# Performance work log

Measured on AMD Instinct MI355X. Metric: run time of the kernel, lower is better.

The kernel has to match this reference:

```python
import jax, jax.numpy as jnp
import numpy as np

B, T, H = 65536, 24, 64  # batch, input_window_size, num_neurons
SLOPE = 25.0             # snntorch fast_sigmoid default slope

@jax.custom_vjp
def spike(x):
    # heaviside forward, fast-sigmoid surrogate backward
    return (x > 0).astype(x.dtype)

def _spike_fwd(x):
    return (x > 0).astype(x.dtype), x

def _spike_bwd(x, g):
    return (g / (SLOPE * jnp.abs(x) + 1.0) ** 2,)

spike.defvjp(_spike_fwd, _spike_bwd)

def slstm_cell(x, syn, mem, Wih, Whh, bih, bhh, thr):
    # snntorch SLSTM: LSTMCell with h=mem, c=syn; reset_mechanism='subtract'
    reset = jax.lax.stop_gradient((mem - thr > 0).astype(x.dtype))
    gates = x @ Wih.T + bih + mem @ Whh.T + bhh  # (B, 4H)
    i, f, g, o = jnp.split(gates, 4, axis=-1)
    syn_new = jax.nn.sigmoid(f) * syn + jax.nn.sigmoid(i) * jnp.tanh(g)
    mem_new = jax.nn.sigmoid(o) * jnp.tanh(syn_new) - reset * thr
    spk = spike(mem_new - thr)
    return spk, syn_new, mem_new

def setup_inputs() -> dict:
    key = jax.random.key(0)
    ks = jax.random.split(key, 11)
    s = float(1.0 / np.sqrt(H))  # LSTMCell uniform init bound
    so = float(1.0 / np.sqrt((T + 2) * H))
    u = lambda k, shape: jax.random.uniform(k, shape, jnp.float32, -s, s)
    return {
        "x": jax.random.normal(ks[0], (B, T, 1), jnp.float32),
        "Wih1": u(ks[1], (4 * H, 1)),
        "Whh1": u(ks[2], (4 * H, H)),
        "bih1": u(ks[3], (4 * H,)),
        "bhh1": u(ks[4], (4 * H,)),
        "thr1": jnp.float32(0.5),
        "Wih2": u(ks[5], (4 * H, H)),
        "Whh2": u(ks[6], (4 * H, H)),
        "bih2": u(ks[7], (4 * H,)),
        "bhh2": u(ks[8], (4 * H,)),
        "thr2": jnp.float32(0.5),
        "Wout": jax.random.uniform(ks[9], (2, (T + 2) * H), jnp.float32, -so, so),
        "bout": jnp.array([0.2, -0.2], jnp.float32),
    }

def reference(x, Wih1, Whh1, bih1, bhh1, thr1,
              Wih2, Whh2, bih2, bhh2, thr2, Wout, bout):
    Bn = x.shape[0]
    Hn = Whh1.shape[1]
    z = jnp.zeros((Bn, Hn), x.dtype)
    carry0 = (z, z, z, z)  # syn1, mem1, syn2, mem2

    def step(carry, xt):
        syn1, mem1, syn2, mem2 = carry
        spk1, syn1, mem1 = slstm_cell(xt, syn1, mem1, Wih1, Whh1, bih1, bhh1, thr1)
        spk2, syn2, mem2 = slstm_cell(spk1, syn2, mem2, Wih2, Whh2, bih2, bhh2, thr2)
        return (syn1, mem1, syn2, mem2), spk2

    (syn1, mem1, syn2, mem2), spk2_seq = jax.lax.scan(
        step, carry0, jnp.swapaxes(x, 0, 1))  # spk2_seq: (T, B, H)
    # extra step: feed mem1 into slstm2
    spk2_last, syn2, mem2 = slstm_cell(mem1, syn2, mem2, Wih2, Whh2, bih2, bhh2, thr2)
    lst = jnp.concatenate(
        [jnp.swapaxes(spk2_seq, 0, 1).reshape(Bn, -1), spk2_last, mem2], axis=1)
    return lst @ Wout.T + bout  # (B, 2)
```

## Files before the change

### kernel.cpp

```cpp
#include <hip/hip_runtime.h>
#include <cstdint>
#include <cstddef>


#define BB 65536
#define TT 24
#define NB 8

typedef float pf2 __attribute__((ext_vector_type(2)));

__device__ __forceinline__ void pk_fma_wlo(pf2& acc, pf2 s, pf2 w) {
  asm("v_pk_fma_f32 %0, %1, %2, %0 op_sel:[0,0,0] op_sel_hi:[1,0,1]"
      : "+v"(acc) : "v"(s), "v"(w));
}
__device__ __forceinline__ void pk_fma_whi(pf2& acc, pf2 s, pf2 w) {
  asm("v_pk_fma_f32 %0, %1, %2, %0 op_sel:[0,1,0] op_sel_hi:[1,1,1]"
      : "+v"(acc) : "v"(s), "v"(w));
}

__device__ __forceinline__ float bcastf(float v, int l) {
  return __int_as_float(__builtin_amdgcn_readlane(__float_as_int(v), l));
}
__device__ __forceinline__ float sigm(float v) {
  return __fdividef(1.0f, 1.0f + __expf(-v));
}
__device__ __forceinline__ float tanh_fast(float v) {
  return fmaf(-2.0f, __fdividef(1.0f, __expf(2.0f * v) + 1.0f), 1.0f);
}
__device__ __forceinline__ float wsum(float v) {
#pragma unroll
  for (int o = 32; o > 0; o >>= 1) v += __shfl_xor(v, o);
  return v;
}

__global__ __attribute__((amdgpu_waves_per_eu(4, 4))) __launch_bounds__(512)
void snn_pass1(
    const float* __restrict__ x, const float* __restrict__ Wih1,
    const float* __restrict__ Whh1, const float* __restrict__ bih1,
    const float* __restrict__ bhh1, const float* __restrict__ thr1p,
    unsigned long long* __restrict__ spk_out, float* __restrict__ mem1_out) {
  __shared__ float4 P1[64][64];
  __shared__ float stM[8][64][NB];
  int tid = threadIdx.x;
  for (int idx = tid; idx < 16384; idx += 512) {
    int k = idx >> 6, m = idx & 63;
    ((float*)&P1[m][k & 63])[k >> 6] = Whh1[idx];
  }
  __syncthreads();
  int lane = tid & 63, wave = tid >> 6;
  int wb = (blockIdx.x * 8 + wave) * NB;
  float thr1 = thr1p[0];
  float b1q[4], wq[4];
#pragma unroll
  for (int q = 0; q < 4; q++) {
    b1q[q] = bih1[q * 64 + lane] + bhh1[q * 64 + lane];
    wq[q] = Wih1[q * 64 + lane];
  }
  float syn[NB], mem[NB];
#pragma unroll
  for (int b = 0; b < NB; b++) { syn[b] = 0.0f; mem[b] = 0.0f; }

  for (int t = 0; t < TT; t++) {
#pragma unroll
    for (int b = 0; b < NB; b++) stM[wave][lane][b] = mem[b];
    unsigned long long myspk = 0;
#pragma unroll
    for (int h = 0; h < 2; h++) {
      const int B0 = h * 4;
      pf2 a2[4][2];
#pragma unroll
      for (int p = 0; p < 2; p++) {
        float x0 = x[(wb + B0 + 2 * p) * TT + t];
        float x1 = x[(wb + B0 + 2 * p + 1) * TT + t];
#pragma unroll
        for (int q = 0; q < 4; q++)
          a2[q][p] = (pf2){fmaf(x0, wq[q], b1q[q]), fmaf(x1, wq[q], b1q[q])};
      }
#pragma unroll 8
      for (int m = 0; m < 64; m++) {
        float4 w = P1[m][lane];
        float4 sa = *(const float4*)&stM[wave][m][B0];
        pf2 s01 = {sa.x, sa.y}, s23 = {sa.z, sa.w};
        pf2 wxy = {w.x, w.y}, wzw = {w.z, w.w};
        pk_fma_wlo(a2[0][0], s01, wxy);
        pk_fma_whi(a2[1][0], s01, wxy);
        pk_fma_wlo(a2[2][0], s01, wzw);
        pk_fma_whi(a2[3][0], s01, wzw);
        pk_fma_wlo(a2[0][1], s23, wxy);
        pk_fma_whi(a2[1][1], s23, wxy);
        pk_fma_wlo(a2[2][1], s23, wzw);
        pk_fma_whi(a2[3][1], s23, wzw);
      }
#pragma unroll
      for (int j = 0; j < 4; j++) {
        int b = B0 + j, p = j >> 1;
        float aq0 = (j & 1) ? a2[0][p].y : a2[0][p].x;
        float aq1 = (j & 1) ? a2[1][p].y : a2[1][p].x;
        float aq2 = (j & 1) ? a2[2][p].y : a2[2][p].x;
        float aq3 = (j & 1) ? a2[3][p].y : a2[3][p].x;
        float ig = sigm(aq0), fg = sigm(aq1);
        float gg = tanh_fast(aq2), og = sigm(aq3);
        float sn = fmaf(fg, syn[b], ig * gg);
        float rst = (mem[b] > thr1) ? thr1 : 0.0f;
        float mn = fmaf(og, tanh_fast(sn), -rst);
        syn[b] = sn;
        mem[b] = mn;
        unsigned long long msk = __ballot(mn > thr1);
        if (lane == b) myspk = msk;
      }
      __builtin_amdgcn_sched_barrier(0);
    }
    if (lane < NB)
      spk_out[(size_t)t * BB + wb + lane] = myspk;
  }
#pragma unroll
  for (int b = 0; b < NB; b++)
    mem1_out[(size_t)(wb + b) * 64 + lane] = mem[b];
}

__global__ __attribute__((amdgpu_waves_per_eu(4, 4))) __launch_bounds__(1024)
void snn_pass2(
    const float* __restrict__ Wih2, const float* __restrict__ Whh2,
    const float* __restrict__ bih2, const float* __restrict__ bhh2,
    const float* __restrict__ thr2p, const float* __restrict__ Wout,
    const float* __restrict__ bout,
    const unsigned long long* __restrict__ spk_in,
    const float* __restrict__ mem1_in, float* __restrict__ out) {
  __shared__ float4 Pih[64][64];
  __shared__ float4 Phh[64][64];
  __shared__ float stM[16][64][NB];
  int tid = threadIdx.x;
  for (int idx = tid; idx < 16384; idx += 1024) {
    int k = idx >> 6, m = idx & 63;
    ((float*)&Pih[m][k & 63])[k >> 6] = Wih2[idx];
    ((float*)&Phh[m][k & 63])[k >> 6] = Whh2[idx];
  }
  __syncthreads();
  int lane = tid & 63, wave = tid >> 6;
  int wb = (blockIdx.x * 16 + wave) * NB;
  float thr2 = thr2p[0];
  float b2q[4];
#pragma unroll
  for (int q = 0; q < 4; q++) b2q[q] = bih2[q * 64 + lane] + bhh2[q * 64 + lane];
  float syn[NB], mem[NB];
  unsigned sb8[NB];
#pragma unroll
  for (int b = 0; b < NB; b++) { syn[b] = 0.0f; mem[b] = 0.0f; sb8[b] = 0u; }

  for (int t = 0; t < TT; t++) {
    unsigned long long mk[NB];
#pragma unroll
    for (int b = 0; b < NB; b++) {
      unsigned long long v = spk_in[(size_t)t * BB + wb + b];
      unsigned lo = __builtin_amdgcn_readfirstlane((unsigned)v);
      unsigned hi = __builtin_amdgcn_readfirstlane((unsigned)(v >> 32));
      mk[b] = ((unsigned long long)hi << 32) | (unsigned long long)lo;
    }
#pragma unroll
    for (int b = 0; b < NB; b++) stM[wave][lane][b] = mem[b];
#pragma unroll
    for (int h = 0; h < 2; h++) {
      const int B0 = h * 4;
      pf2 a2[4][2];
#pragma unroll
      for (int q = 0; q < 4; q++) {
#pragma unroll
        for (int p = 0; p < 2; p++) a2[q][p] = (pf2){b2q[q], b2q[q]};
      }
#pragma unroll 8
      for (int m = 0; m < 64; m++) {
        float4 wh = Phh[m][lane];
        float4 sa = *(const float4*)&stM[wave][m][B0];
        pf2 s01 = {sa.x, sa.y}, s23 = {sa.z, sa.w};
        pf2 wxy = {wh.x, wh.y}, wzw = {wh.z, wh.w};
        pk_fma_wlo(a2[0][0], s01, wxy);
        pk_fma_whi(a2[1][0], s01, wxy);
        pk_fma_wlo(a2[2][0], s01, wzw);
        pk_fma_whi(a2[3][0], s01, wzw);
        pk_fma_wlo(a2[0][1], s23, wxy);
        pk_fma_whi(a2[1][1], s23, wxy);
        pk_fma_wlo(a2[2][1], s23, wzw);
        pk_fma_whi(a2[3][1], s23, wzw);
      }
#pragma unroll
      for (int j = 0; j < 4; j++) {
        int b = B0 + j, p = j >> 1;
        unsigned long long k = mk[b];
        while (__builtin_popcountll(k) >= 4) {
          int m0 = __builtin_ctzll(k); k &= k - 1;
          int m1 = __builtin_ctzll(k); k &= k - 1;
          int m2 = __builtin_ctzll(k); k &= k - 1;
          int m3 = __builtin_ctzll(k); k &= k - 1;
          float4 r0 = Pih[m0][lane];
          float4 r1 = Pih[m1][lane];
          float4 r2 = Pih[m2][lane];
          float4 r3 = Pih[m3][lane];
          if ((j & 1) == 0) {
            a2[0][p].x += r0.x; a2[1][p].x += r0.y; a2[2][p].x += r0.z; a2[3][p].x += r0.w;
            a2[0][p].x += r1.x; a2[1][p].x += r1.y; a2[2][p].x += r1.z; a2[3][p].x += r1.w;
            a2[0][p].x += r2.x; a2[1][p].x += r2.y; a2[2][p].x += r2.z; a2[3][p].x += r2.w;
            a2[0][p].x += r3.x; a2[1][p].x += r3.y; a2[2][p].x += r3.z; a2[3][p].x += r3.w;
          } else {
            a2[0][p].y += r0.x; a2[1][p].y += r0.y; a2[2][p].y += r0.z; a2[3][p].y += r0.w;
            a2[0][p].y += r1.x; a2[1][p].y += r1.y; a2[2][p].y += r1.z; a2[3][p].y += r1.w;
            a2[0][p].y += r2.x; a2[1][p].y += r2.y; a2[2][p].y += r2.z; a2[3][p].y += r2.w;
            a2[0][p].y += r3.x; a2[1][p].y += r3.y; a2[2][p].y += r3.z; a2[3][p].y += r3.w;
          }
        }
        while (k) {
          int m0 = __builtin_ctzll(k); k &= k - 1;
          float4 r0 = Pih[m0][lane];
          if ((j & 1) == 0) {
            a2[0][p].x += r0.x; a2[1][p].x += r0.y; a2[2][p].x += r0.z; a2[3][p].x += r0.w;
          } else {
            a2[0][p].y += r0.x; a2[1][p].y += r0.y; a2[2][p].y += r0.z; a2[3][p].y += r0.w;
          }
        }
        float aq0 = (j & 1) ? a2[0][p].y : a2[0][p].x;
        float aq1 = (j & 1) ? a2[1][p].y : a2[1][p].x;
        float aq2 = (j & 1) ? a2[2][p].y : a2[2][p].x;
        float aq3 = (j & 1) ? a2[3][p].y : a2[3][p].x;
        float ig = sigm(aq0), fg = sigm(aq1);
        float gg = tanh_fast(aq2), og = sigm(aq3);
        float sn = fmaf(fg, syn[b], ig * gg);
        float rst = (mem[b] > thr2) ? thr2 : 0.0f;
        float mn = fmaf(og, tanh_fast(sn), -rst);
        syn[b] = sn;
        mem[b] = mn;
        sb8[b] |= (mn > thr2) ? (1u << t) : 0u;
      }
      __builtin_amdgcn_sched_barrier(0);
    }
  }

  float m1[NB];
#pragma unroll
  for (int b = 0; b < NB; b++) m1[b] = mem1_in[(size_t)(wb + b) * 64 + lane];
  float acc[NB][4];
#pragma unroll
  for (int b = 0; b < NB; b++) {
#pragma unroll
    for (int q = 0; q < 4; q++) acc[b][q] = b2q[q];
  }
#pragma unroll 4
  for (int m = 0; m < 64; m++) {
    float4 wi = Pih[m][lane];
    float4 wh = Phh[m][lane];
#pragma unroll
    for (int b = 0; b < NB; b++) {
      float s1 = bcastf(m1[b], m);
      float s2 = bcastf(mem[b], m);
      acc[b][0] = fmaf(s1, wi.x, fmaf(s2, wh.x, acc[b][0]));
      acc[b][1] = fmaf(s1, wi.y, fmaf(s2, wh.y, acc[b][1]));
      acc[b][2] = fmaf(s1, wi.z, fmaf(s2, wh.z, acc[b][2]));
      acc[b][3] = fmaf(s1, wi.w, fmaf(s2, wh.w, acc[b][3]));
    }
  }
  float p0[NB], p1[NB];
#pragma unroll
  for (int b = 0; b < NB; b++) { p0[b] = 0.0f; p1[b] = 0.0f; }
#pragma unroll 4
  for (int t = 0; t < TT; t++) {
    float w0 = Wout[t * 64 + lane];
    float w1 = Wout[1664 + t * 64 + lane];
#pragma unroll
    for (int b = 0; b < NB; b++) {
      float sf = ((sb8[b] >> t) & 1u) ? 1.0f : 0.0f;
      p0[b] = fmaf(sf, w0, p0[b]);
      p1[b] = fmaf(sf, w1, p1[b]);
    }
  }
  float wA0 = Wout[1536 + lane], wA1 = Wout[1664 + 1536 + lane];
  float wB0 = Wout[1600 + lane], wB1 = Wout[1664 + 1600 + lane];
  float bo0 = bout[0], bo1 = bout[1];
#pragma unroll
  for (int b = 0; b < NB; b++) {
    float ig = sigm(acc[b][0]), fg = sigm(acc[b][1]);
    float gg = tanh_fast(acc[b][2]), og = sigm(acc[b][3]);
    float sn = fmaf(fg, syn[b], ig * gg);
    float rst = (mem[b] > thr2) ? thr2 : 0.0f;
    float mn = fmaf(og, tanh_fast(sn), -rst);
    float sf = (mn > thr2) ? 1.0f : 0.0f;
    p0[b] = fmaf(sf, wA0, p0[b]);
    p1[b] = fmaf(sf, wA1, p1[b]);
    p0[b] = fmaf(mn, wB0, p0[b]);
    p1[b] = fmaf(mn, wB1, p1[b]);
  }
  float vout = 0.0f;
#pragma unroll
  for (int b = 0; b < NB; b++) {
    float r0 = wsum(p0[b]);
    float r1 = wsum(p1[b]);
    if (lane == 2 * b) vout = r0;
    if (lane == 2 * b + 1) vout = r1;
  }
  if (lane < 2 * NB)
    out[(size_t)wb * 2 + lane] = vout + ((lane & 1) ? bo1 : bo0);
}

extern "C" void kernel_launch(void* const* d_in, const int* in_sizes, int n_in,
                              void* d_out, int out_size, void* d_ws, size_t ws_size,
                              hipStream_t stream) {
  const float* x = (const float*)d_in[0];
  const float* Wih1 = (const float*)d_in[1];
  const float* Whh1 = (const float*)d_in[2];
  const float* bih1 = (const float*)d_in[3];
  const float* bhh1 = (const float*)d_in[4];
  const float* thr1 = (const float*)d_in[5];
  const float* Wih2 = (const float*)d_in[6];
  const float* Whh2 = (const float*)d_in[7];
  const float* bih2 = (const float*)d_in[8];
  const float* bhh2 = (const float*)d_in[9];
  const float* thr2 = (const float*)d_in[10];
  const float* Wout = (const float*)d_in[11];
  const float* bout = (const float*)d_in[12];

  unsigned long long* spk = (unsigned long long*)d_ws;
  float* mem1 = (float*)((char*)d_ws + (size_t)TT * BB * 8);

  snn_pass1<<<BB / (8 * NB), 512, 0, stream>>>(x, Wih1, Whh1, bih1, bhh1, thr1,
                                               spk, mem1);
  snn_pass2<<<BB / (16 * NB), 1024, 0, stream>>>(Wih2, Whh2, bih2, bhh2, thr2,
                                                 Wout, bout, spk, mem1,
                                                 (float*)d_out);
}
```

Baseline: 1.776 ms.

## Move half of Whh1 and all of Wih2 weight tables from LDS to global memory

Adds a setup kernel that pre-packs Whh1 and Wih2 into float4-interleaved global buffers. Pass1 now keeps only half of the Whh1 table in LDS and streams the other half from global or cache. Pass2 drops its Pih LDS table and reads Wih2 rows straight from global memory. The goal is to free LDS so more blocks or waves fit per CU, at the cost of global and L1/L2 latency on the inner loops. It also removes the occupancy attribute from pass1 and adds one extra kernel launch.

```diff
diff --git a/kernel.cpp b/kernel.cpp
--- a/kernel.cpp
+++ b/kernel.cpp
@@ -33,18 +33,30 @@
   return v;
 }
 
-__global__ __attribute__((amdgpu_waves_per_eu(4, 4))) __launch_bounds__(512)
-void snn_pass1(
+__global__ void snn_setup(const float* __restrict__ Whh1,
+                          const float* __restrict__ Wih2,
+                          float* __restrict__ P1G, float* __restrict__ PihG) {
+  int idx = blockIdx.x * blockDim.x + threadIdx.x;
+  if (idx < 16384) {
+    int k = idx >> 6, m = idx & 63;
+    int q = k >> 6, j = k & 63;
+    P1G[(m * 64 + j) * 4 + q] = Whh1[idx];
+    PihG[(m * 64 + j) * 4 + q] = Wih2[idx];
+  }
+}
+
+__global__ __launch_bounds__(512) void snn_pass1(
     const float* __restrict__ x, const float* __restrict__ Wih1,
     const float* __restrict__ Whh1, const float* __restrict__ bih1,
     const float* __restrict__ bhh1, const float* __restrict__ thr1p,
+    const float4* __restrict__ P1G,
     unsigned long long* __restrict__ spk_out, float* __restrict__ mem1_out) {
-  __shared__ float4 P1[64][64];
+  __shared__ float4 P1[32][64];
   __shared__ float stM[8][64][NB];
   int tid = threadIdx.x;
   for (int idx = tid; idx < 16384; idx += 512) {
     int k = idx >> 6, m = idx & 63;
-    ((float*)&P1[m][k & 63])[k >> 6] = Whh1[idx];
+    if (m < 32) ((float*)&P1[m][k & 63])[k >> 6] = Whh1[idx];
   }
   __syncthreads();
   int lane = tid & 63, wave = tid >> 6;
@@ -77,8 +89,23 @@
           a2[q][p] = (pf2){fmaf(x0, wq[q], b1q[q]), fmaf(x1, wq[q], b1q[q])};
       }
 #pragma unroll 8
-      for (int m = 0; m < 64; m++) {
+      for (int m = 0; m < 32; m++) {
         float4 w = P1[m][lane];
+        float4 sa = *(const float4*)&stM[wave][m][B0];
+        pf2 s01 = {sa.x, sa.y}, s23 = {sa.z, sa.w};
+        pf2 wxy = {w.x, w.y}, wzw = {w.z, w.w};
+        pk_fma_wlo(a2[0][0], s01, wxy);
+        pk_fma_whi(a2[1][0], s01, wxy);
+        pk_fma_wlo(a2[2][0], s01, wzw);
+        pk_fma_whi(a2[3][0], s01, wzw);
+        pk_fma_wlo(a2[0][1], s23, wxy);
+        pk_fma_whi(a2[1][1], s23, wxy);
+        pk_fma_wlo(a2[2][1], s23, wzw);
+        pk_fma_whi(a2[3][1], s23, wzw);
+      }
+#pragma unroll 8
+      for (int m = 32; m < 64; m++) {
+        float4 w = P1G[m * 64 + lane];
         float4 sa = *(const float4*)&stM[wave][m][B0];
         pf2 s01 = {sa.x, sa.y}, s23 = {sa.z, sa.w};
         pf2 wxy = {w.x, w.y}, wzw = {w.z, w.w};
@@ -123,16 +150,14 @@
     const float* __restrict__ Wih2, const float* __restrict__ Whh2,
     const float* __restrict__ bih2, const float* __restrict__ bhh2,
     const float* __restrict__ thr2p, const float* __restrict__ Wout,
-    const float* __restrict__ bout,
+    const float* __restrict__ bout, const float4* __restrict__ PihG,
     const unsigned long long* __restrict__ spk_in,
     const float* __restrict__ mem1_in, float* __restrict__ out) {
-  __shared__ float4 Pih[64][64];
   __shared__ float4 Phh[64][64];
   __shared__ float stM[16][64][NB];
   int tid = threadIdx.x;
   for (int idx = tid; idx < 16384; idx += 1024) {
     int k = idx >> 6, m = idx & 63;
-    ((float*)&Pih[m][k & 63])[k >> 6] = Wih2[idx];
     ((float*)&Phh[m][k & 63])[k >> 6] = Whh2[idx];
   }
   __syncthreads();
@@ -191,10 +216,10 @@
           int m1 = __builtin_ctzll(k); k &= k - 1;
           int m2 = __builtin_ctzll(k); k &= k - 1;
           int m3 = __builtin_ctzll(k); k &= k - 1;
-          float4 r0 = Pih[m0][lane];
-          float4 r1 = Pih[m1][lane];
-          float4 r2 = Pih[m2][lane];
-          float4 r3 = Pih[m3][lane];
+          float4 r0 = PihG[m0 * 64 + lane];
+          float4 r1 = PihG[m1 * 64 + lane];
+          float4 r2 = PihG[m2 * 64 + lane];
+          float4 r3 = PihG[m3 * 64 + lane];
           if ((j & 1) == 0) {
             a2[0][p].x += r0.x; a2[1][p].x += r0.y; a2[2][p].x += r0.z; a2[3][p].x += r0.w;
             a2[0][p].x += r1.x; a2[1][p].x += r1.y; a2[2][p].x += r1.z; a2[3][p].x += r1.w;
@@ -209,7 +234,7 @@
         }
         while (k) {
           int m0 = __builtin_ctzll(k); k &= k - 1;
-          float4 r0 = Pih[m0][lane];
+          float4 r0 = PihG[m0 * 64 + lane];
           if ((j & 1) == 0) {
             a2[0][p].x += r0.x; a2[1][p].x += r0.y; a2[2][p].x += r0.z; a2[3][p].x += r0.w;
           } else {
@@ -244,7 +269,7 @@
   }
 #pragma unroll 4
   for (int m = 0; m < 64; m++) {
-    float4 wi = Pih[m][lane];
+    float4 wi = PihG[m * 64 + lane];
     float4 wh = Phh[m][lane];
 #pragma unroll
     for (int b = 0; b < NB; b++) {
@@ -317,10 +342,13 @@
 
   unsigned long long* spk = (unsigned long long*)d_ws;
   float* mem1 = (float*)((char*)d_ws + (size_t)TT * BB * 8);
-
+  float* P1G = (float*)((char*)d_ws + (size_t)TT * BB * 8 + (size_t)BB * 64 * 4);
+  float* PihG = P1G + 16384;
+
+  snn_setup<<<32, 512, 0, stream>>>(Whh1, Wih2, P1G, PihG);
   snn_pass1<<<BB / (8 * NB), 512, 0, stream>>>(x, Wih1, Whh1, bih1, bhh1, thr1,
-                                               spk, mem1);
+                                               (const float4*)P1G, spk, mem1);
   snn_pass2<<<BB / (16 * NB), 1024, 0, stream>>>(Wih2, Whh2, bih2, bhh2, thr2,
-                                                 Wout, bout, spk, mem1,
-                                                 (float*)d_out);
-}
+                                                 Wout, bout, (const float4*)PihG,
+                                                 spk, mem1, (float*)d_out);
+}
```

After: 1.871 ms. +5.3%, slower.

## Fuse both SLSTM layers into one kernel and read Wih2 from global memory

Applied to the files above, without the earlier changes.

The two passes are merged into a single kernel. Each wave now computes layer-1 and layer-2 per timestep with all state held in registers, so the spike masks and mem1 no longer round-trip through global memory. A small setup kernel writes Wih2 into a gate-interleaved global layout, and the spike-driven row gathers read from there instead of LDS. This keeps LDS at two weight tables (Whh1, Whh2) plus the state buffer at 1024 threads per block. The cost is that the sparse Wih2 lookups now go through the cache hierarchy rather than LDS, and each thread carries more live registers.

```diff
diff --git a/kernel.cpp b/kernel.cpp
--- a/kernel.cpp
+++ b/kernel.cpp
@@ -33,37 +33,56 @@
   return v;
 }
 
-__global__ __attribute__((amdgpu_waves_per_eu(4, 4))) __launch_bounds__(512)
-void snn_pass1(
+__global__ void snn_setup(const float* __restrict__ Wih2,
+                          float* __restrict__ PihG) {
+  int idx = blockIdx.x * blockDim.x + threadIdx.x;
+  if (idx < 16384) {
+    int k = idx >> 6, m = idx & 63;
+    int q = k >> 6, j = k & 63;
+    PihG[(m * 64 + j) * 4 + q] = Wih2[idx];
+  }
+}
+
+__global__ __attribute__((amdgpu_waves_per_eu(4, 4))) __launch_bounds__(1024)
+void snn_fused(
     const float* __restrict__ x, const float* __restrict__ Wih1,
     const float* __restrict__ Whh1, const float* __restrict__ bih1,
     const float* __restrict__ bhh1, const float* __restrict__ thr1p,
-    unsigned long long* __restrict__ spk_out, float* __restrict__ mem1_out) {
+    const float* __restrict__ Whh2, const float* __restrict__ bih2,
+    const float* __restrict__ bhh2, const float* __restrict__ thr2p,
+    const float* __restrict__ Wout, const float* __restrict__ bout,
+    const float4* __restrict__ PihG, float* __restrict__ out) {
   __shared__ float4 P1[64][64];
-  __shared__ float stM[8][64][NB];
+  __shared__ float4 Phh[64][64];
+  __shared__ float stM[16][64][NB];
   int tid = threadIdx.x;
-  for (int idx = tid; idx < 16384; idx += 512) {
+  for (int idx = tid; idx < 16384; idx += 1024) {
     int k = idx >> 6, m = idx & 63;
     ((float*)&P1[m][k & 63])[k >> 6] = Whh1[idx];
+    ((float*)&Phh[m][k & 63])[k >> 6] = Whh2[idx];
   }
   __syncthreads();
   int lane = tid & 63, wave = tid >> 6;
-  int wb = (blockIdx.x * 8 + wave) * NB;
-  float thr1 = thr1p[0];
-  float b1q[4], wq[4];
+  int wb = (blockIdx.x * 16 + wave) * NB;
+  float thr1 = thr1p[0], thr2 = thr2p[0];
+  float b1q[4], wq[4], b2q[4];
 #pragma unroll
   for (int q = 0; q < 4; q++) {
     b1q[q] = bih1[q * 64 + lane] + bhh1[q * 64 + lane];
     wq[q] = Wih1[q * 64 + lane];
-  }
-  float syn[NB], mem[NB];
-#pragma unroll
-  for (int b = 0; b < NB; b++) { syn[b] = 0.0f; mem[b] = 0.0f; }
+    b2q[q] = bih2[q * 64 + lane] + bhh2[q * 64 + lane];
+  }
+  float syn1[NB], mem1[NB], syn2[NB], mem2[NB];
+  unsigned sb8[NB];
+#pragma unroll
+  for (int b = 0; b < NB; b++) {
+    syn1[b] = 0.0f; mem1[b] = 0.0f; syn2[b] = 0.0f; mem2[b] = 0.0f; sb8[b] = 0u;
+  }
 
   for (int t = 0; t < TT; t++) {
 #pragma unroll
-    for (int b = 0; b < NB; b++) stM[wave][lane][b] = mem[b];
-    unsigned long long myspk = 0;
+    for (int b = 0; b < NB; b++) stM[wave][lane][b] = mem1[b];
+    unsigned long long mk[NB];
 #pragma unroll
     for (int h = 0; h < 2; h++) {
       const int B0 = h * 4;
@@ -100,64 +119,17 @@
         float aq3 = (j & 1) ? a2[3][p].y : a2[3][p].x;
         float ig = sigm(aq0), fg = sigm(aq1);
         float gg = tanh_fast(aq2), og = sigm(aq3);
-        float sn = fmaf(fg, syn[b], ig * gg);
-        float rst = (mem[b] > thr1) ? thr1 : 0.0f;
+        float sn = fmaf(fg, syn1[b], ig * gg);
+        float rst = (mem1[b] > thr1) ? thr1 : 0.0f;
         float mn = fmaf(og, tanh_fast(sn), -rst);
-        syn[b] = sn;
-        mem[b] = mn;
-        unsigned long long msk = __ballot(mn > thr1);
-        if (lane == b) myspk = msk;
+        syn1[b] = sn;
+        mem1[b] = mn;
+        mk[b] = __ballot(mn > thr1);
       }
       __builtin_amdgcn_sched_barrier(0);
     }
-    if (lane < NB)
-      spk_out[(size_t)t * BB + wb + lane] = myspk;
-  }
-#pragma unroll
-  for (int b = 0; b < NB; b++)
-    mem1_out[(size_t)(wb + b) * 64 + lane] = mem[b];
-}
-
-__global__ __attribute__((amdgpu_waves_per_eu(4, 4))) __launch_bounds__(1024)
-void snn_pass2(
-    const float* __restrict__ Wih2, const float* __restrict__ Whh2,
-    const float* __restrict__ bih2, const float* __restrict__ bhh2,
-    const float* __restrict__ thr2p, const float* __restrict__ Wout,
-    const float* __restrict__ bout,
-    const unsigned long long* __restrict__ spk_in,
-    const float* __restrict__ mem1_in, float* __restrict__ out) {
-  __shared__ float4 Pih[64][64];
-  __shared__ float4 Phh[64][64];
-  __shared__ float stM[16][64][NB];
-  int tid = threadIdx.x;
-  for (int idx = tid; idx < 16384; idx += 1024) {
-    int k = idx >> 6, m = idx & 63;
-    ((float*)&Pih[m][k & 63])[k >> 6] = Wih2[idx];
-    ((float*)&Phh[m][k & 63])[k >> 6] = Whh2[idx];
-  }
-  __syncthreads();
-  int lane = tid & 63, wave = tid >> 6;
-  int wb = (blockIdx.x * 16 + wave) * NB;
-  float thr2 = thr2p[0];
-  float b2q[4];
-#pragma unroll
-  for (int q = 0; q < 4; q++) b2q[q] = bih2[q * 64 + lane] + bhh2[q * 64 + lane];
-  float syn[NB], mem[NB];
-  unsigned sb8[NB];
-#pragma unroll
-  for (int b = 0; b < NB; b++) { syn[b] = 0.0f; mem[b] = 0.0f; sb8[b] = 0u; }
-
-  for (int t = 0; t < TT; t++) {
-    unsigned long long mk[NB];
-#pragma unroll
-    for (int b = 0; b < NB; b++) {
-      unsigned long long v = spk_in[(size_t)t * BB + wb + b];
-      unsigned lo = __builtin_amdgcn_readfirstlane((unsigned)v);
-      unsigned hi = __builtin_amdgcn_readfirstlane((unsigned)(v >> 32));
-      mk[b] = ((unsigned long long)hi << 32) | (unsigned long long)lo;
-    }
-#pragma unroll
-    for (int b = 0; b < NB; b++) stM[wave][lane][b] = mem[b];
+#pragma unroll
+    for (int b = 0; b < NB; b++) stM[wave][lane][b] = mem2[b];
 #pragma unroll
     for (int h = 0; h < 2; h++) {
       const int B0 = h * 4;
@@ -191,10 +163,10 @@
           int m1 = __builtin_ctzll(k); k &= k - 1;
           int m2 = __builtin_ctzll(k); k &= k - 1;
           int m3 = __builtin_ctzll(k); k &= k - 1;
-          float4 r0 = Pih[m0][lane];
-          float4 r1 = Pih[m1][lane];
-          float4 r2 = Pih[m2][lane];
-          float4 r3 = Pih[m3][lane];
+          float4 r0 = PihG[m0 * 64 + lane];
+          float4 r1 = PihG[m1 * 64 + lane];
+          float4 r2 = PihG[m2 * 64 + lane];
+          float4 r3 = PihG[m3 * 64 + lane];
           if ((j & 1) == 0) {
             a2[0][p].x += r0.x; a2[1][p].x += r0.y; a2[2][p].x += r0.z; a2[3][p].x += r0.w;
             a2[0][p].x += r1.x; a2[1][p].x += r1.y; a2[2][p].x += r1.z; a2[3][p].x += r1.w;
@@ -209,7 +181,7 @@
         }
         while (k) {
           int m0 = __builtin_ctzll(k); k &= k - 1;
-          float4 r0 = Pih[m0][lane];
+          float4 r0 = PihG[m0 * 64 + lane];
           if ((j & 1) == 0) {
             a2[0][p].x += r0.x; a2[1][p].x += r0.y; a2[2][p].x += r0.z; a2[3][p].x += r0.w;
           } else {
@@ -222,20 +194,17 @@
         float aq3 = (j & 1) ? a2[3][p].y : a2[3][p].x;
         float ig = sigm(aq0), fg = sigm(aq1);
         float gg = tanh_fast(aq2), og = sigm(aq3);
-        float sn = fmaf(fg, syn[b], ig * gg);
-        float rst = (mem[b] > thr2) ? thr2 : 0.0f;
+        float sn = fmaf(fg, syn2[b], ig * gg);
+        float rst = (mem2[b] > thr2) ? thr2 : 0.0f;
         float mn = fmaf(og, tanh_fast(sn), -rst);
-        syn[b] = sn;
-        mem[b] = mn;
+        syn2[b] = sn;
+        mem2[b] = mn;
         sb8[b] |= (mn > thr2) ? (1u << t) : 0u;
       }
       __builtin_amdgcn_sched_barrier(0);
     }
   }
 
-  float m1[NB];
-#pragma unroll
-  for (int b = 0; b < NB; b++) m1[b] = mem1_in[(size_t)(wb + b) * 64 + lane];
   float acc[NB][4];
 #pragma unroll
   for (int b = 0; b < NB; b++) {
@@ -244,12 +213,12 @@
   }
 #pragma unroll 4
   for (int m = 0; m < 64; m++) {
-    float4 wi = Pih[m][lane];
+    float4 wi = PihG[m * 64 + lane];
     float4 wh = Phh[m][lane];
 #pragma unroll
     for (int b = 0; b < NB; b++) {
-      float s1 = bcastf(m1[b], m);
-      float s2 = bcastf(mem[b], m);
+      float s1 = bcastf(mem1[b], m);
+      float s2 = bcastf(mem2[b], m);
       acc[b][0] = fmaf(s1, wi.x, fmaf(s2, wh.x, acc[b][0]));
       acc[b][1] = fmaf(s1, wi.y, fmaf(s2, wh.y, acc[b][1]));
       acc[b][2] = fmaf(s1, wi.z, fmaf(s2, wh.z, acc[b][2]));
@@ -277,8 +246,8 @@
   for (int b = 0; b < NB; b++) {
     float ig = sigm(acc[b][0]), fg = sigm(acc[b][1]);
     float gg = tanh_fast(acc[b][2]), og = sigm(acc[b][3]);
-    float sn = fmaf(fg, syn[b], ig * gg);
-    float rst = (mem[b] > thr2) ? thr2 : 0.0f;
+    float sn = fmaf(fg, syn2[b], ig * gg);
+    float rst = (mem2[b] > thr2) ? thr2 : 0.0f;
     float mn = fmaf(og, tanh_fast(sn), -rst);
     float sf = (mn > thr2) ? 1.0f : 0.0f;
     p0[b] = fmaf(sf, wA0, p0[b]);
@@ -315,12 +284,10 @@
   const float* Wout = (const float*)d_in[11];
   const float* bout = (const float*)d_in[12];
 
-  unsigned long long* spk = (unsigned long long*)d_ws;
-  float* mem1 = (float*)((char*)d_ws + (size_t)TT * BB * 8);
-
-  snn_pass1<<<BB / (8 * NB), 512, 0, stream>>>(x, Wih1, Whh1, bih1, bhh1, thr1,
-                                               spk, mem1);
-  snn_pass2<<<BB / (16 * NB), 1024, 0, stream>>>(Wih2, Whh2, bih2, bhh2, thr2,
-                                                 Wout, bout, spk, mem1,
-                                                 (float*)d_out);
-}
+  float* PihG = (float*)d_ws;
+
+  snn_setup<<<32, 512, 0, stream>>>(Wih2, PihG);
+  snn_fused<<<BB / (16 * NB), 1024, 0, stream>>>(
+      x, Wih1, Whh1, bih1, bhh1, thr1, Whh2, bih2, bhh2, thr2, Wout, bout,
+      (const float4*)PihG, (float*)d_out);
+}
```

Measured after the change: 1.858 ms. +4.6%, slower.
